# Kernel optimization log

Measured on AMD Instinct MI355X. Metric: run time of the kernel, lower is better.

Reference implementation:

```python
import jax, jax.numpy as jnp
import numpy as np

D = 256      # layer_size
BLOCK = 4096 # block_size


def setup_inputs() -> dict:
    key = jax.random.key(0)
    ks = jax.random.split(key, 7)
    B, T = 4, BLOCK
    x = jax.random.normal(ks[0], (B, T, D), dtype=jnp.float32)
    s = 1.0 / np.sqrt(D)
    Wq = jax.random.uniform(ks[1], (D, D), jnp.float32, -s, s)
    bq = jax.random.uniform(ks[2], (D,), jnp.float32, -s, s)
    Wk = jax.random.uniform(ks[3], (D, D), jnp.float32, -s, s)
    bk = jax.random.uniform(ks[4], (D,), jnp.float32, -s, s)
    Wv = jax.random.uniform(ks[5], (D, D), jnp.float32, -s, s)
    bv = jax.random.uniform(ks[6], (D,), jnp.float32, -s, s)
    return {"x": x, "Wq": Wq, "bq": bq, "Wk": Wk, "bk": bk, "Wv": Wv, "bv": bv}


def reference(x, Wq, bq, Wk, bk, Wv, bv):
    # x: [B, T, D]; Linear uses x @ W.T + b (torch convention)
    B, T, _ = x.shape
    Q = x @ Wq.T + bq
    K = x @ Wk.T + bk
    V = x @ Wv.T + bv
    scores = jnp.einsum('btd,bsd->bts', Q, K) / jnp.sqrt(jnp.float32(D))  # [B,T,T]
    # causal mask buffer is [1,1,T,T]; torch masked_fill broadcasts it against
    # [B,T,T] scores, yielding [1,B,T,T] — reproduce that shape faithfully.
    causal = jnp.tril(jnp.ones((T, T), dtype=bool))[None, None]  # [1,1,T,T]
    scores = jnp.where(causal, scores, -jnp.inf)                 # [1,B,T,T]
    attn = jax.nn.softmax(scores, axis=-1)                       # [1,B,T,T]
    out = jnp.einsum('abts,bsd->abtd', attn, V)                  # [1,B,T,D]
    return out
```

## Files before the change

### kernel.cpp

```cpp
#include <hip/hip_runtime.h>
#include <hip/hip_bf16.h>

typedef __attribute__((ext_vector_type(8))) short short8;
typedef __attribute__((ext_vector_type(4))) short short4v;
typedef __attribute__((ext_vector_type(4))) float f32x4;

#define MFMA16(a, b, c) __builtin_amdgcn_mfma_f32_16x16x32_bf16(a, b, c, 0, 0, 0)

__device__ __forceinline__ short f2bf(float f) {
    union { float f; unsigned u; } v; v.f = f;
    unsigned r = v.u + 0x7fffu + ((v.u >> 16) & 1u);
    return (short)(r >> 16);
}
__device__ __forceinline__ unsigned pack2(float lo, float hi) {
    return ((unsigned)(unsigned short)f2bf(hi) << 16) |
           (unsigned)(unsigned short)f2bf(lo);
}
__device__ __forceinline__ void gload16(const void* g, void* lds) {
    __builtin_amdgcn_global_load_lds(
        (const __attribute__((address_space(1))) unsigned int*)g,
        (__attribute__((address_space(3))) unsigned int*)lds, 16, 0, 0);
}

__global__ __launch_bounds__(256) void wconv(
    const float* __restrict__ Wq, const float* __restrict__ Wk,
    const float* __restrict__ Wv, short* __restrict__ Wb)
{
    int e = (blockIdx.x * 256 + threadIdx.x) * 8;
    const float* p = (e < 65536) ? (Wq + e)
                   : (e < 131072) ? (Wk + (e - 65536))
                                  : (Wv + (e - 131072));
    float4 a = *(const float4*)p;
    float4 b = *(const float4*)(p + 4);
    short8 h = { f2bf(a.x), f2bf(a.y), f2bf(a.z), f2bf(a.w),
                 f2bf(b.x), f2bf(b.y), f2bf(b.z), f2bf(b.w) };
    *(short8*)(Wb + e) = h;
}

__global__ __launch_bounds__(256) void qkv_proj(
    const float* __restrict__ x, const short* __restrict__ Wb,
    const float* __restrict__ bq, const float* __restrict__ bk,
    const float* __restrict__ bv,
    short* __restrict__ Qb, short* __restrict__ Kb, short* __restrict__ VTg)
{
    __shared__ short xs[64 * 264];
    __shared__ short wsS[64 * 264];

    const int tid = threadIdx.x;
    const int wid = tid >> 6;
    const int l   = tid & 63;
    const int l15 = l & 15, lg = l >> 4;
    const int r0  = blockIdx.x * 64;
    const int cg  = blockIdx.y;

    {
        const float4* src = (const float4*)(x + (size_t)r0 * 256);
        #pragma unroll
        for (int p = 0; p < 16; ++p) {
            float4 v = src[p * 256 + tid];
            int idx = (p * 256 + tid) * 4;
            int row = idx >> 8, col = idx & 255;
            short4v h = { f2bf(v.x), f2bf(v.y), f2bf(v.z), f2bf(v.w) };
            *(short4v*)&xs[row * 264 + col] = h;
        }
    }

    short8 wreg[8];
    {
        const short8* wsrc = (const short8*)(Wb + (size_t)(cg * 3) * 64 * 256);
        #pragma unroll
        for (int p = 0; p < 8; ++p) wreg[p] = wsrc[p * 256 + tid];
    }
    __syncthreads();

    short8 afr[8];
    {
        const int arow = wid * 16 + l15;
        #pragma unroll
        for (int ks = 0; ks < 8; ++ks)
            afr[ks] = *(const short8*)&xs[arow * 264 + ks * 32 + lg * 8];
    }

    const float* bm[3] = { bq, bk, bv };

    for (int c = 0; c < 3; ++c) {
        const int gc  = cg * 3 + c;
        const int m   = gc >> 2;
        const int wr0 = (gc & 3) * 64;

        #pragma unroll
        for (int p = 0; p < 8; ++p) {
            int idx8 = p * 256 + tid;
            int row = idx8 >> 5, col = (idx8 & 31) * 8;
            *(short8*)&wsS[row * 264 + col] = wreg[p];
        }
        __syncthreads();

        if (c < 2) {
            const short8* wsrc =
                (const short8*)(Wb + (size_t)(gc + 1) * 64 * 256);
            #pragma unroll
            for (int p = 0; p < 8; ++p) wreg[p] = wsrc[p * 256 + tid];
        }

        f32x4 acc[4] = {};
        #pragma unroll
        for (int n = 0; n < 4; ++n) {
            const short* kr = &wsS[(n * 16 + l15) * 264 + lg * 8];
            #pragma unroll
            for (int ks = 0; ks < 8; ++ks) {
                short8 bfr = *(const short8*)(kr + ks * 32);
                acc[n] = MFMA16(afr[ks], bfr, acc[n]);
            }
        }

        const int rowbase = r0 + wid * 16 + (lg << 2);
        #pragma unroll
        for (int n = 0; n < 4; ++n) {
            const int col   = wr0 + n * 16 + l15;
            const float bias = bm[m][col];
            #pragma unroll
            for (int j = 0; j < 4; ++j) {
                const int grow = rowbase + j;
                short hv = f2bf(acc[n][j] + bias);
                if (m == 0)      Qb[(size_t)grow * 256 + col] = hv;
                else if (m == 1) Kb[(size_t)grow * 256 + col] = hv;
                else {
                    int bb = grow >> 12, tt = grow & 4095;
                    VTg[(size_t)bb * (256 * 4096) + (size_t)col * 4096 + tt] = hv;
                }
            }
        }
        __syncthreads();
    }
}

__global__ __launch_bounds__(256, 2) void attn_fwd(
    const short* __restrict__ Qb, const short* __restrict__ Kb,
    const short* __restrict__ VTg, float* __restrict__ out)
{
    __shared__ __attribute__((aligned(16))) char SMEM[71680];
    short* KV = (short*)SMEM;
    short* Ps = (short*)(SMEM + 65536);

    const int tid = threadIdx.x;
    const int wid = tid >> 6;
    const int l   = tid & 63;
    const int l15 = l & 15, lg = l >> 4;
    const int rg  = wid >> 1;
    const int par = wid & 1;

    const int bid = blockIdx.x;
    const int xcd = bid & 7;
    const int b   = xcd & 3, hh = xcd >> 2;
    const int jj  = bid >> 3;
    const int rowblk = (jj < 32) ? (2 * jj + hh) : (127 - (2 * (jj - 32) + hh));
    const int nkt = rowblk + 1;
    const int nsi = (nkt + 1) >> 1;

    const short* KbB = Kb  + (size_t)b * 4096 * 256;
    const short* VTB = VTg + (size_t)b * (256 * 4096);

    const int qrow_loc = rg * 16 + l15;
    const int qrow     = rowblk * 32 + qrow_loc;

    short8 qf[8];
    {
        const short* qr = Qb + ((size_t)(b * 4096 + qrow)) * 256 + lg * 8;
        #pragma unroll
        for (int ks = 0; ks < 8; ++ks)
            qf[ks] = *(const short8*)(qr + ks * 32);
    }

    auto stage = [&](int si) {
        const int ktt = 2 * si + (wid & 1);
        if (ktt >= nkt) return;
        if (wid < 2) {
            char* lb = (char*)SMEM + (wid & 1) * 16384;
            const short* gK = KbB + (size_t)ktt * 32 * 256;
            #pragma unroll
            for (int inst = 0; inst < 16; ++inst) {
                int off  = inst * 1024 + l * 16;
                int key  = off >> 9;
                int slot = ((off >> 4) & 31) ^ (key & 15);
                gload16(gK + key * 256 + slot * 8, lb + inst * 1024);
            }
        } else {
            char* lb = (char*)SMEM + 32768 + (wid & 1) * 16384;
            const short* gV = VTB + ktt * 32;
            #pragma unroll
            for (int inst = 0; inst < 16; ++inst) {
                int off = inst * 1024 + l * 16;
                int d   = off >> 6;
                int s   = ((off >> 4) & 3) ^ ((d >> 1) & 3);
                gload16(gV + (size_t)d * 4096 + s * 8, lb + inst * 1024);
            }
        }
    };
    stage(0);

    f32x4 o[16] = {};
    float mrow = -INFINITY, srow = 0.f;

    for (int si = 0; si < nsi; ++si) {
        asm volatile("s_waitcnt vmcnt(0)" ::: "memory");
        __syncthreads();

        const int kt  = 2 * si + par;
        const bool act = (kt < nkt);
        short8 vf2[4], pb;
        float  f;

        if (act) {
            const short* Kt = (const short*)(SMEM + par * 16384);
            f32x4 sA[2] = {};
            #pragma unroll
            for (int tk = 0; tk < 2; ++tk) {
                const int key = tk * 16 + l15;
                #pragma unroll
                for (int ks = 0; ks < 8; ++ks) {
                    const int slot = (ks * 4 + lg) ^ l15;
                    short8 kf = *(const short8*)(Kt + key * 256 + slot * 8);
                    sA[tk] = MFMA16(kf, qf[ks], sA[tk]);
                }
            }

            float pmax = -INFINITY;
            #pragma unroll
            for (int tk = 0; tk < 2; ++tk)
                #pragma unroll
                for (int j4 = 0; j4 < 4; ++j4) {
                    const int key = kt * 32 + tk * 16 + lg * 4 + j4;
                    float v = sA[tk][j4] * 0.0625f;
                    v = (key > qrow) ? -INFINITY : v;
                    sA[tk][j4] = v;
                    pmax = fmaxf(pmax, v);
                }
            pmax = fmaxf(pmax, __shfl_xor(pmax, 16, 64));
            pmax = fmaxf(pmax, __shfl_xor(pmax, 32, 64));

            const float mn  = fmaxf(mrow, pmax);
            const float mne = (mn == -INFINITY) ? 0.f : mn;
            f = __expf(mrow - mne);
            mrow = mn;

            short* Pw = Ps + wid * 768;
            float ps = 0.f;
            #pragma unroll
            for (int tk = 0; tk < 2; ++tk) {
                float p0 = __expf(sA[tk][0] - mne);
                float p1 = __expf(sA[tk][1] - mne);
                float p2 = __expf(sA[tk][2] - mne);
                float p3 = __expf(sA[tk][3] - mne);
                ps += (p0 + p1) + (p2 + p3);
                unsigned* pw = (unsigned*)(Pw + l15 * 48 + tk * 16 + lg * 4);
                pw[0] = pack2(p0, p1);
                pw[1] = pack2(p2, p3);
            }
            srow = srow * f + ps;

            asm volatile("s_waitcnt lgkmcnt(0)" ::: "memory");
            __builtin_amdgcn_sched_barrier(0);

            pb = *(const short8*)(Pw + l15 * 48 + lg * 8);

            const short* Vt = (const short*)(SMEM + 32768 + par * 16384);
            #pragma unroll
            for (int dt = 0; dt < 12; ++dt) {
                #pragma unroll
                for (int j4 = 0; j4 < 4; ++j4) o[dt][j4] *= f;
                const int d  = dt * 16 + l15;
                const int sx = lg ^ ((d >> 1) & 3);
                short8 va = *(const short8*)(Vt + d * 32 + sx * 8);
                o[dt] = MFMA16(va, pb, o[dt]);
            }
            #pragma unroll
            for (int dt = 12; dt < 16; ++dt) {
                const int d  = dt * 16 + l15;
                const int sx = lg ^ ((d >> 1) & 3);
                vf2[dt - 12] = *(const short8*)(Vt + d * 32 + sx * 8);
            }
        }

        __syncthreads();
        if (si + 1 < nsi) stage(si + 1);
        __builtin_amdgcn_sched_barrier(0);

        if (act) {
            #pragma unroll
            for (int dt = 12; dt < 16; ++dt) {
                #pragma unroll
                for (int j4 = 0; j4 < 4; ++j4) o[dt][j4] *= f;
                o[dt] = MFMA16(vf2[dt - 12], pb, o[dt]);
            }
        }
    }

    srow += __shfl_xor(srow, 16, 64);
    srow += __shfl_xor(srow, 32, 64);

    __syncthreads();
    float* scr = (float*)SMEM;
    float* ms  = (float*)(SMEM + 33280);

    if (par == 1) {
        #pragma unroll
        for (int dt = 0; dt < 16; ++dt)
            *(f32x4*)&scr[qrow_loc * 260 + dt * 16 + lg * 4] = o[dt];
        if (lg == 0) {
            ms[qrow_loc * 2 + 0] = mrow;
            ms[qrow_loc * 2 + 1] = srow;
        }
    }
    __syncthreads();
    if (par == 0) {
        const float m1 = ms[qrow_loc * 2 + 0];
        const float s1 = ms[qrow_loc * 2 + 1];
        const float M  = fmaxf(mrow, m1);
        const float w0 = __expf(mrow - M);
        const float w1 = __expf(m1 - M);
        const float rs = 1.f / (srow * w0 + s1 * w1);
        float* og = out + ((size_t)(b * 4096 + qrow)) * 256;
        #pragma unroll
        for (int dt = 0; dt < 16; ++dt) {
            f32x4 o1 = *(f32x4*)&scr[qrow_loc * 260 + dt * 16 + lg * 4];
            f32x4 r;
            #pragma unroll
            for (int j4 = 0; j4 < 4; ++j4)
                r[j4] = (o[dt][j4] * w0 + o1[j4] * w1) * rs;
            *(f32x4*)&og[dt * 16 + lg * 4] = r;
        }
    }
}

extern "C" void kernel_launch(void* const* d_in, const int* in_sizes, int n_in,
                              void* d_out, int out_size, void* d_ws, size_t ws_size,
                              hipStream_t stream) {
    const float* x  = (const float*)d_in[0];
    const float* Wq = (const float*)d_in[1];
    const float* bq = (const float*)d_in[2];
    const float* Wk = (const float*)d_in[3];
    const float* bk = (const float*)d_in[4];
    const float* Wv = (const float*)d_in[5];
    const float* bv = (const float*)d_in[6];

    short* Qb  = (short*)d_ws;
    short* Kb  = Qb + (size_t)16384 * 256;
    short* VTg = Kb + (size_t)16384 * 256;
    short* Wb  = VTg + (size_t)4 * 256 * 4096;
    float* out = (float*)d_out;

    wconv<<<dim3(96), dim3(256), 0, stream>>>(Wq, Wk, Wv, Wb);
    qkv_proj<<<dim3(256, 4), dim3(256), 0, stream>>>(x, Wb, bq, bk, bv,
                                                     Qb, Kb, VTg);
    attn_fwd<<<dim3(512), dim3(256), 0, stream>>>(Qb, Kb, VTg, out);
}
```

Before: 161.9 us.

## Split attention key tiles four ways per block with 512-thread blocks and tree merge

The attention kernel moves from 256-thread blocks with a two-way split over key tiles to 512-thread blocks where four wave groups each take every fourth key tile. Partial softmax states are merged in two rounds through shared memory, with a guard for rows whose max is still negative infinity. The grid now runs heavy row blocks first with a simple batch interleave, replacing the previous XCD-aware pairing. The aim is to halve the serial key-loop length per block and improve latency hiding. The cost is doubled shared memory (about 140 KB, so one block per CU), an extra merge round, and idle waves on the short causal rows.

```diff
diff --git a/kernel.cpp b/kernel.cpp
--- a/kernel.cpp
+++ b/kernel.cpp
@@ -135,28 +135,25 @@
     }
 }
 
-__global__ __launch_bounds__(256, 2) void attn_fwd(
+__global__ __launch_bounds__(512, 1) void attn_fwd(
     const short* __restrict__ Qb, const short* __restrict__ Kb,
     const short* __restrict__ VTg, float* __restrict__ out)
 {
-    __shared__ __attribute__((aligned(16))) char SMEM[71680];
-    short* KV = (short*)SMEM;
-    short* Ps = (short*)(SMEM + 65536);
+    __shared__ __attribute__((aligned(16))) char SMEM[143360];
+    short* Ps = (short*)(SMEM + 131072);
 
     const int tid = threadIdx.x;
     const int wid = tid >> 6;
     const int l   = tid & 63;
     const int l15 = l & 15, lg = l >> 4;
-    const int rg  = wid >> 1;
-    const int par = wid & 1;
-
-    const int bid = blockIdx.x;
-    const int xcd = bid & 7;
-    const int b   = xcd & 3, hh = xcd >> 2;
-    const int jj  = bid >> 3;
-    const int rowblk = (jj < 32) ? (2 * jj + hh) : (127 - (2 * (jj - 32) + hh));
-    const int nkt = rowblk + 1;
-    const int nsi = (nkt + 1) >> 1;
+    const int rg  = wid >> 2;
+    const int par = wid & 3;
+
+    const int bid    = blockIdx.x;
+    const int rowblk = 127 - (bid >> 2);
+    const int b      = bid & 3;
+    const int nkt    = rowblk + 1;
+    const int nsi    = (nkt + 3) >> 2;
 
     const short* KbB = Kb  + (size_t)b * 4096 * 256;
     const short* VTB = VTg + (size_t)b * (256 * 4096);
@@ -173,10 +170,10 @@
     }
 
     auto stage = [&](int si) {
-        const int ktt = 2 * si + (wid & 1);
+        const int ktt = si * 4 + (wid & 3);
         if (ktt >= nkt) return;
-        if (wid < 2) {
-            char* lb = (char*)SMEM + (wid & 1) * 16384;
+        if (wid < 4) {
+            char* lb = SMEM + (wid & 3) * 16384;
             const short* gK = KbB + (size_t)ktt * 32 * 256;
             #pragma unroll
             for (int inst = 0; inst < 16; ++inst) {
@@ -186,7 +183,7 @@
                 gload16(gK + key * 256 + slot * 8, lb + inst * 1024);
             }
         } else {
-            char* lb = (char*)SMEM + 32768 + (wid & 1) * 16384;
+            char* lb = SMEM + 65536 + (wid & 3) * 16384;
             const short* gV = VTB + ktt * 32;
             #pragma unroll
             for (int inst = 0; inst < 16; ++inst) {
@@ -206,7 +203,7 @@
         asm volatile("s_waitcnt vmcnt(0)" ::: "memory");
         __syncthreads();
 
-        const int kt  = 2 * si + par;
+        const int kt  = si * 4 + par;
         const bool act = (kt < nkt);
         short8 vf2[4], pb;
         float  f;
@@ -264,7 +261,7 @@
 
             pb = *(const short8*)(Pw + l15 * 48 + lg * 8);
 
-            const short* Vt = (const short*)(SMEM + 32768 + par * 16384);
+            const short* Vt = (const short*)(SMEM + 65536 + par * 16384);
             #pragma unroll
             for (int dt = 0; dt < 12; ++dt) {
                 #pragma unroll
@@ -301,29 +298,61 @@
 
     __syncthreads();
     float* scr = (float*)SMEM;
-    float* ms  = (float*)(SMEM + 33280);
-
+    float* ms  = (float*)(SMEM + 66560);
+
+    const int rl = rg * 16 + l15;
+
+    if (par >= 2) {
+        const int p = par - 2;
+        #pragma unroll
+        for (int dt = 0; dt < 16; ++dt)
+            *(f32x4*)&scr[p * 8320 + rl * 260 + dt * 16 + lg * 4] = o[dt];
+        if (lg == 0) {
+            ms[p * 64 + rl * 2 + 0] = mrow;
+            ms[p * 64 + rl * 2 + 1] = srow;
+        }
+    }
+    __syncthreads();
+    if (par < 2) {
+        const float m1 = ms[par * 64 + rl * 2 + 0];
+        const float s1 = ms[par * 64 + rl * 2 + 1];
+        const float M  = fmaxf(mrow, m1);
+        const float Me = (M == -INFINITY) ? 0.f : M;
+        const float w0 = __expf(mrow - Me);
+        const float w1 = __expf(m1 - Me);
+        srow = srow * w0 + s1 * w1;
+        mrow = M;
+        #pragma unroll
+        for (int dt = 0; dt < 16; ++dt) {
+            f32x4 o1 = *(f32x4*)&scr[par * 8320 + rl * 260 + dt * 16 + lg * 4];
+            #pragma unroll
+            for (int j4 = 0; j4 < 4; ++j4)
+                o[dt][j4] = o[dt][j4] * w0 + o1[j4] * w1;
+        }
+    }
+    __syncthreads();
     if (par == 1) {
         #pragma unroll
         for (int dt = 0; dt < 16; ++dt)
-            *(f32x4*)&scr[qrow_loc * 260 + dt * 16 + lg * 4] = o[dt];
+            *(f32x4*)&scr[rl * 260 + dt * 16 + lg * 4] = o[dt];
         if (lg == 0) {
-            ms[qrow_loc * 2 + 0] = mrow;
-            ms[qrow_loc * 2 + 1] = srow;
+            ms[rl * 2 + 0] = mrow;
+            ms[rl * 2 + 1] = srow;
         }
     }
     __syncthreads();
     if (par == 0) {
-        const float m1 = ms[qrow_loc * 2 + 0];
-        const float s1 = ms[qrow_loc * 2 + 1];
+        const float m1 = ms[rl * 2 + 0];
+        const float s1 = ms[rl * 2 + 1];
         const float M  = fmaxf(mrow, m1);
-        const float w0 = __expf(mrow - M);
-        const float w1 = __expf(m1 - M);
+        const float Me = (M == -INFINITY) ? 0.f : M;
+        const float w0 = __expf(mrow - Me);
+        const float w1 = __expf(m1 - Me);
         const float rs = 1.f / (srow * w0 + s1 * w1);
-        float* og = out + ((size_t)(b * 4096 + qrow)) * 256;
+        float* og = out + ((size_t)(b * 4096 + rowblk * 32 + rl)) * 256;
         #pragma unroll
         for (int dt = 0; dt < 16; ++dt) {
-            f32x4 o1 = *(f32x4*)&scr[qrow_loc * 260 + dt * 16 + lg * 4];
+            f32x4 o1 = *(f32x4*)&scr[rl * 260 + dt * 16 + lg * 4];
             f32x4 r;
             #pragma unroll
             for (int j4 = 0; j4 < 4; ++j4)
@@ -353,5 +382,5 @@
     wconv<<<dim3(96), dim3(256), 0, stream>>>(Wq, Wk, Wv, Wb);
     qkv_proj<<<dim3(256, 4), dim3(256), 0, stream>>>(x, Wb, bq, bk, bv,
                                                      Qb, Kb, VTg);
-    attn_fwd<<<dim3(512), dim3(256), 0, stream>>>(Qb, Kb, VTg, out);
-}
+    attn_fwd<<<dim3(512), dim3(512), 0, stream>>>(Qb, Kb, VTg, out);
+}
```

Result: faster. 144.6 us, median of 2 (-10.7%).
